# Optimization experiments

Hardware: AMD Instinct MI355X
Metric: run time of the kernel (lower is better)

## Reference

```python
import jax, jax.numpy as jnp
import numpy as np

COMMITMENT_COST = 0.25


def setup_inputs() -> dict:
    key = jax.random.key(0)
    k1, k2 = jax.random.split(key)
    ze = jax.random.normal(k1, (16, 256, 32, 32), dtype=jnp.float32)
    codebook = jax.random.normal(k2, (8192, 256), dtype=jnp.float32) * 0.02
    return {"ze": ze, "codebook": codebook}


def reference(ze, codebook):
    # ze: [B, C, H, W] -> [B, H, W, C]
    B, C, H, W = ze.shape
    ze_nhwc = jnp.transpose(ze, (0, 2, 3, 1))
    ze_flat = ze_nhwc.reshape(B * H * W, C)

    # squared L2 distances to every codebook row: [B*H*W, vocab]
    distances = (
        jnp.sum(ze_flat ** 2, axis=1, keepdims=True)
        + jnp.sum(codebook ** 2, axis=1)
        - 2.0 * ze_flat @ codebook.T
    )
    encoding_indices = jnp.argmin(distances, axis=1)  # [B*H*W]
    zq = codebook[encoding_indices].reshape(B, H, W, C)

    sg = jax.lax.stop_gradient
    quantization_loss = jnp.mean((sg(ze_nhwc) - zq) ** 2)
    commitment_loss = jnp.mean((ze_nhwc - sg(zq)) ** 2)
    vq_loss = quantization_loss + COMMITMENT_COST * commitment_loss

    # straight-through estimator (training mode)
    zq = ze_nhwc + sg(zq - ze_nhwc)
    zq = jnp.transpose(zq, (0, 3, 1, 2))  # back to [B, C, H, W]
    return vq_loss, zq, encoding_indices.reshape(B, H * W)
```

## Files before the change

### kernel.cpp

```cpp
#include <hip/hip_runtime.h>
#include <hip/hip_bf16.h>

#define NPIX 16384
#define NVOC 8192
#define CHUNK 32

typedef short short8v __attribute__((ext_vector_type(8)));
typedef float floatx4 __attribute__((ext_vector_type(4)));

#define WS_ZEBF   0u
#define WS_BLIST  0u
#define WS_PART   0u
#define WS_CBBF   8388608u
#define WS_PK     8388608u
#define WS_TAU    8519680u
#define WS_ZEF    12582912u
#define WS_MIN    29360128u
#define WS_BN     37748736u
#define WS_AN     37781504u
#define WS_BCNT   37847040u
#define WS_BMAXU  37847552u
#define WS_QCNT   37847556u
#define WS_QUEUE  37847808u

__device__ __forceinline__ short f2bf(float v) {
  __bf16 h = (__bf16)v;
  return __builtin_bit_cast(short, h);
}

__device__ __forceinline__ unsigned long long packdj(float d, int j) {
  return ((unsigned long long)__float_as_uint(d) << 32) | (unsigned int)j;
}

__device__ __forceinline__ void gll16(const void* g, void* l) {
  __builtin_amdgcn_global_load_lds(
      (const __attribute__((address_space(1))) void*)g,
      (__attribute__((address_space(3))) void*)l, 16, 0, 0);
}

__device__ __forceinline__ float np_pairwise128_sq(const float* x, int stride) {
  float r[8];
#pragma unroll
  for (int j = 0; j < 8; ++j) {
    float v = x[j * stride];
    r[j] = __fmul_rn(v, v);
  }
#pragma unroll
  for (int i = 1; i < 16; ++i) {
#pragma unroll
    for (int j = 0; j < 8; ++j) {
      float v = x[(i * 8 + j) * stride];
      r[j] = __fadd_rn(r[j], __fmul_rn(v, v));
    }
  }
  return __fadd_rn(__fadd_rn(__fadd_rn(r[0], r[1]), __fadd_rn(r[2], r[3])),
                   __fadd_rn(__fadd_rn(r[4], r[5]), __fadd_rn(r[6], r[7])));
}

__global__ __launch_bounds__(256) void k_bnorm(const float* __restrict__ cb,
                                               float* __restrict__ bn,
                                               unsigned* __restrict__ bmaxu) {
  __shared__ float rows[64][257];
  int tid = threadIdx.x;
  int c0 = blockIdx.x * 64;
  for (int r = 0; r < 64; ++r)
    rows[r][tid] = cb[(size_t)(c0 + r) * 256 + tid];
  __syncthreads();
  if (tid < 64) {
    float a = np_pairwise128_sq(&rows[tid][0], 1);
    float b = np_pairwise128_sq(&rows[tid][128], 1);
    float v = __fadd_rn(a, b);
    bn[c0 + tid] = v;
    atomicMax(bmaxu, __float_as_uint(v));
  }
}

__global__ __launch_bounds__(256) void k_cvt_ze(const float* __restrict__ ze,
                                                short* __restrict__ zebff,
                                                float* __restrict__ zef,
                                                float* __restrict__ an) {
  __shared__ float t[64][132];
  int tid = threadIdx.x;
  int p0 = blockIdx.x * 64;
  int b = p0 >> 10, hw0 = p0 & 1023;
  const float* src = ze + (size_t)b * 262144 + hw0;
  float apart = 0.f;
  for (int half = 0; half < 2; ++half) {
    if (half) __syncthreads();
    {
      int hw = tid & 63, cq = tid >> 6;
#pragma unroll
      for (int i = 0; i < 32; ++i) {
        int cl = i * 4 + cq;
        t[hw][cl] = src[(size_t)(half * 128 + cl) * 1024 + hw];
      }
    }
    __syncthreads();
    {
      int r = tid >> 2, cg = tid & 3;
      float* fd = zef + (size_t)(p0 + r) * 256 + half * 128 + cg * 32;
#pragma unroll
      for (int s = 0; s < 8; ++s) {
        float4 v = *reinterpret_cast<const float4*>(&t[r][cg * 32 + s * 4]);
        *reinterpret_cast<float4*>(fd + s * 4) = v;
      }
    }
    {
      int pg_l = tid >> 6, l = tid & 63;
      size_t pg = (size_t)(p0 >> 4) + pg_l;
      int lr = l & 15, lg = l >> 4;
#pragma unroll
      for (int kl = 0; kl < 4; ++kl) {
        int ks = half * 4 + kl;
        short8v v8;
#pragma unroll
        for (int e = 0; e < 8; ++e)
          v8[e] = f2bf(t[pg_l * 16 + lr][kl * 32 + lg * 8 + e]);
        *reinterpret_cast<short8v*>(zebff + (pg * 8 + ks) * 512 + l * 8) = v8;
      }
    }
    if (tid < 64) {
      float a = np_pairwise128_sq(&t[tid][0], 1);
      apart = half ? __fadd_rn(apart, a) : a;
    }
  }
  if (tid < 64) an[p0 + tid] = apart;
}

__global__ __launch_bounds__(256) void k_cvt_cb(const float* __restrict__ cb,
                                                short* __restrict__ cbbft,
                                                unsigned* __restrict__ bmaxu,
                                                int* __restrict__ qcnt) {
  __shared__ short t[64][264];
  int tid = threadIdx.x;
  if (blockIdx.x == 0 && tid == 0) {
    bmaxu[0] = 0u;
    qcnt[0] = 0;
  }
  int j0 = blockIdx.x * 64;
  {
    int col = tid >> 2, q = tid & 3;
    const float* src = cb + (size_t)(j0 + col) * 256 + q * 64;
#pragma unroll
    for (int i = 0; i < 8; ++i) {
      float4 a = *reinterpret_cast<const float4*>(src + i * 8);
      float4 b = *reinterpret_cast<const float4*>(src + i * 8 + 4);
      short8v v;
      v[0] = f2bf(a.x); v[1] = f2bf(a.y); v[2] = f2bf(a.z); v[3] = f2bf(a.w);
      v[4] = f2bf(b.x); v[5] = f2bf(b.y); v[6] = f2bf(b.z); v[7] = f2bf(b.w);
      *reinterpret_cast<short8v*>(&t[col][q * 64 + i * 8]) = v;
    }
  }
  __syncthreads();
  short* dst = cbbft + (size_t)blockIdx.x * 16384;
#pragma unroll
  for (int s = 0; s < 8; ++s) {
    int cid = tid + s * 256;
    int kc = cid >> 6, c2 = cid & 63;
    short8v v = *reinterpret_cast<const short8v*>(&t[c2][kc * 8]);
    *reinterpret_cast<short8v*>(dst + cid * 8) = v;
  }
}

__global__ __launch_bounds__(256, 2) void k_gemm(const short* __restrict__ zebff,
                                                 const short* __restrict__ cbbft,
                                                 const float* __restrict__ bn,
                                                 float* __restrict__ wsmin) {
  __shared__ short lds[32768];
  __shared__ float bnlds[1024];
  int tid = threadIdx.x;
  int lane = tid & 63, w = tid >> 6;
  int g = lane >> 4, r16 = lane & 15;
  int oct = blockIdx.x & 7, chunk = blockIdx.x >> 3;
  int p0 = chunk * 256;
  int ncol0 = oct * 1024;

  short8v pix[4][8];
  {
    const short* base = zebff + ((size_t)(p0 >> 4) + w * 4) * 4096 + lane * 8;
#pragma unroll
    for (int pf = 0; pf < 4; ++pf)
#pragma unroll
      for (int ks = 0; ks < 8; ++ks)
        pix[pf][ks] =
            *reinterpret_cast<const short8v*>(base + pf * 4096 + ks * 512);
  }
  gll16(bn + ncol0 + tid * 4, &bnlds[tid * 4]);

#define STAGE(t, boff)                                                         \
  {                                                                            \
    const short* src_ = cbbft + (size_t)(oct * 16 + (t)) * 16384;              \
    _Pragma("unroll") for (int s = 0; s < 8; ++s) {                            \
      int cid_ = tid + s * 256;                                                \
      gll16(src_ + cid_ * 8, &lds[(boff) + cid_ * 8]);                         \
    }                                                                          \
  }
  STAGE(0, 0)
  asm volatile("s_waitcnt vmcnt(0)" ::: "memory");
  __builtin_amdgcn_s_barrier();

  float* wbase = wsmin + (size_t)(oct * 16) * NPIX + p0 + w * 64 + r16;

  for (int t = 0; t < 16; ++t) {
    int bA = (t & 1) * 16384;
    int bC = bA ^ 16384;
    if (t < 15) STAGE(t + 1, bC)
    float4 bnv[4];
#pragma unroll
    for (int cf = 0; cf < 4; ++cf)
      bnv[cf] =
          *reinterpret_cast<const float4*>(&bnlds[t * 64 + cf * 16 + g * 4]);
    floatx4 acc[4][4];
#pragma unroll
    for (int cf = 0; cf < 4; ++cf)
#pragma unroll
      for (int pf = 0; pf < 4; ++pf) acc[cf][pf] = floatx4{0.f, 0.f, 0.f, 0.f};
    __builtin_amdgcn_s_setprio(1);
#pragma unroll
    for (int ks = 0; ks < 8; ++ks) {
      short8v cfr[4];
#pragma unroll
      for (int cf = 0; cf < 4; ++cf)
        cfr[cf] = *reinterpret_cast<const short8v*>(
            &lds[bA + (((ks * 4 + g) * 64) + cf * 16 + r16) * 8]);
#pragma unroll
      for (int cf = 0; cf < 4; ++cf)
#pragma unroll
        for (int pf = 0; pf < 4; ++pf)
          acc[cf][pf] = __builtin_amdgcn_mfma_f32_16x16x32_bf16(
              cfr[cf], pix[pf][ks], acc[cf][pf], 0, 0, 0);
    }
    __builtin_amdgcn_s_setprio(0);
    float pmin[4];
#pragma unroll
    for (int pf = 0; pf < 4; ++pf) {
      float m_ = 3.4e38f;
#pragma unroll
      for (int cf = 0; cf < 4; ++cf)
#pragma unroll
        for (int rr = 0; rr < 4; ++rr)
          m_ = fminf(m_, __builtin_fmaf(-2.0f, acc[cf][pf][rr], bnv[cf][rr]));
      m_ = fminf(m_, __shfl_xor(m_, 16));
      m_ = fminf(m_, __shfl_xor(m_, 32));
      pmin[pf] = m_;
    }
    if (lane < 16) {
#pragma unroll
      for (int pf = 0; pf < 4; ++pf)
        wbase[(size_t)t * NPIX + pf * 16] = pmin[pf];
    }
    asm volatile("s_waitcnt vmcnt(0)" ::: "memory");
    __builtin_amdgcn_s_barrier();
  }
#undef STAGE
}

__global__ __launch_bounds__(256) void k_tau(const float* __restrict__ wsmin,
                                             const float* __restrict__ an,
                                             const unsigned* __restrict__ bmaxu,
                                             float* __restrict__ tau,
                                             unsigned long long* __restrict__ pk) {
  __shared__ float sm[4][64];
  int tid = threadIdx.x;
  int px = tid & 63, q = tid >> 6;
  int p = blockIdx.x * 64 + px;
  float m0 = 3.4e38f, m1 = 3.4e38f, m2 = 3.4e38f, m3 = 3.4e38f;
#pragma unroll
  for (int i = 0; i < 8; ++i) {
    int c = q * 32 + i * 4;
    m0 = fminf(m0, wsmin[(size_t)c * NPIX + p]);
    m1 = fminf(m1, wsmin[(size_t)(c + 1) * NPIX + p]);
    m2 = fminf(m2, wsmin[(size_t)(c + 2) * NPIX + p]);
    m3 = fminf(m3, wsmin[(size_t)(c + 3) * NPIX + p]);
  }
  sm[q][px] = fminf(fminf(m0, m1), fminf(m2, m3));
  __syncthreads();
  if (tid < 64) {
    float m = fminf(fminf(sm[0][tid], sm[1][tid]), fminf(sm[2][tid], sm[3][tid]));
    float bmaxf = sqrtf(__uint_as_float(bmaxu[0]));
    tau[p] = m + 0.017f * sqrtf(an[p]) * bmaxf + 2e-4f;
    pk[p] = ~0ull;
  }
}

__global__ __launch_bounds__(256) void k_compact(const float* __restrict__ wsmin,
                                                 const float* __restrict__ tau,
                                                 int* __restrict__ bcnt,
                                                 int* __restrict__ blist,
                                                 int* __restrict__ qcnt,
                                                 int* __restrict__ queue) {
  __shared__ int wbase[4];
  __shared__ int running;
  int c = blockIdx.x;
  const float* row = wsmin + (size_t)c * NPIX;
  int* dst = blist + (size_t)c * NPIX;
  int tid = threadIdx.x;
  int lane = tid & 63, wv = tid >> 6;
  if (tid == 0) running = 0;
  __syncthreads();
  for (int base = 0; base < NPIX; base += 256) {
    int p = base + tid;
    bool flag = row[p] <= tau[p];
    unsigned long long mask = __ballot(flag);
    int cnt = __popcll(mask);
    int pre = __popcll(mask & ((1ull << lane) - 1ull));
    if (lane == 0) wbase[wv] = cnt;
    __syncthreads();
    if (tid == 0) {
      int r = running;
#pragma unroll
      for (int w2 = 0; w2 < 4; ++w2) {
        int t = wbase[w2];
        wbase[w2] = r;
        r += t;
      }
      running = r;
    }
    __syncthreads();
    if (flag) dst[wbase[wv] + pre] = p;
    __syncthreads();
  }
  if (tid == 0) {
    int n = running;
    bcnt[c] = n;
    int nch = (n + CHUNK - 1) / CHUNK;
    if (nch > 0) {
      int q0 = atomicAdd(qcnt, nch);
      for (int i = 0; i < nch; ++i) queue[q0 + i] = c | (i << 16);
    }
  }
}

__global__ __launch_bounds__(256) void k_rescore_b(
    const float* __restrict__ zef, const float* __restrict__ cb,
    const float* __restrict__ an, const float* __restrict__ bn,
    const int* __restrict__ bcnt, const int* __restrict__ blist,
    const int* __restrict__ qcnt, const int* __restrict__ queue,
    unsigned long long* __restrict__ pk) {
  __shared__ float cst[64][257];
  __shared__ float zl[32][264];
  __shared__ int pidx[32];
  __shared__ float apx[32];
  int tid = threadIdx.x;
  int lane = tid & 63, wv = tid >> 6;
  int nq = qcnt[0];
  for (int qi = blockIdx.x; qi < nq; qi += 256) {
    int e = queue[qi];
    int c = e & 0xffff;
    int chunk = e >> 16;
    int n = bcnt[c];
    int base = chunk * CHUNK;
    int cnt_here = min(CHUNK, n - base);
    __syncthreads();
    {
      int col = tid >> 2, kq = tid & 3;
      const float* src = cb + (size_t)(c * 64 + col) * 256 + kq * 64;
#pragma unroll
      for (int i = 0; i < 16; ++i) {
        float4 v = *reinterpret_cast<const float4*>(src + i * 4);
        *reinterpret_cast<float4*>(&cst[col][kq * 64 + i * 4]) = v;
      }
    }
    {
      int px = tid >> 3, seg = tid & 7;
      int idx = base + min(px, cnt_here - 1);
      int p = blist[(size_t)c * NPIX + idx];
      const float* src = zef + (size_t)p * 256 + seg * 32;
#pragma unroll
      for (int i = 0; i < 8; ++i) {
        float4 v = *reinterpret_cast<const float4*>(src + i * 4);
        *reinterpret_cast<float4*>(&zl[px][seg * 32 + i * 4]) = v;
      }
      if (seg == 0) {
        pidx[px] = p;
        apx[px] = an[p];
      }
    }
    __syncthreads();
    int j_global = c * 64 + lane;
    float bnj = bn[j_global];
    float acc[8];
#pragma unroll
    for (int i = 0; i < 8; ++i) acc[i] = 0.f;
#pragma unroll 4
    for (int k4 = 0; k4 < 64; ++k4) {
      float4 cv = *reinterpret_cast<const float4*>(&cst[lane][k4 * 4]);
#pragma unroll
      for (int i = 0; i < 8; ++i) {
        float4 zv =
            *reinterpret_cast<const float4*>(&zl[wv * 8 + i][k4 * 4]);
        acc[i] = __builtin_fmaf(zv.x, cv.x, acc[i]);
        acc[i] = __builtin_fmaf(zv.y, cv.y, acc[i]);
        acc[i] = __builtin_fmaf(zv.z, cv.z, acc[i]);
        acc[i] = __builtin_fmaf(zv.w, cv.w, acc[i]);
      }
    }
#pragma unroll
    for (int i = 0; i < 8; ++i) {
      int px = wv * 8 + i;
      float d = __fsub_rn(__fadd_rn(apx[px], bnj), 2.0f * acc[i]);
      unsigned long long q = packdj(d, j_global);
#pragma unroll
      for (int off = 1; off < 64; off <<= 1) {
        unsigned long long q2 = __shfl_xor(q, off);
        q = q2 < q ? q2 : q;
      }
      if (lane == 0) atomicMin(&pk[pidx[px]], q);
    }
  }
}

__global__ __launch_bounds__(256) void k_gather(const float* __restrict__ ze,
                                                const float* __restrict__ cb,
                                                const unsigned long long* __restrict__ pk,
                                                float* __restrict__ out_zq,
                                                float* __restrict__ out_idx,
                                                float* __restrict__ part) {
  __shared__ float qrow[64][257];
  __shared__ int sidx[64];
  int tid = threadIdx.x;
  int p0 = blockIdx.x * 64;
  int b = p0 >> 10, hw0 = p0 & 1023;
  if (tid < 64) {
    int bi = (int)(unsigned int)(pk[p0 + tid] & 0xffffffffull);
    sidx[tid] = bi;
    out_idx[p0 + tid] = (float)bi;
  }
  __syncthreads();
  for (int r = 0; r < 64; ++r)
    qrow[r][tid] = cb[(size_t)sidx[r] * 256 + tid];
  __syncthreads();
  float lsum = 0.f;
  size_t zbase = (size_t)b * 262144 + hw0;
#pragma unroll 4
  for (int i = 0; i < 64; ++i) {
    int px = tid & 63;
    int c = i * 4 + (tid >> 6);
    float qv = qrow[px][c];
    size_t gi = zbase + (size_t)c * 1024 + px;
    float zev = ze[gi];
    out_zq[gi] = __fadd_rn(zev, __fsub_rn(qv, zev));
    float d = zev - qv;
    lsum = __builtin_fmaf(d, d, lsum);
  }
#pragma unroll
  for (int off = 32; off; off >>= 1) lsum += __shfl_xor(lsum, off, 64);
  __shared__ float wsum[4];
  if ((tid & 63) == 0) wsum[tid >> 6] = lsum;
  __syncthreads();
  if (tid == 0) part[blockIdx.x] = (wsum[0] + wsum[1]) + (wsum[2] + wsum[3]);
}

__global__ __launch_bounds__(256) void k_final(const float* __restrict__ part,
                                               float* __restrict__ out0) {
  int tid = threadIdx.x;
  float s = part[tid];
#pragma unroll
  for (int off = 32; off; off >>= 1) s += __shfl_xor(s, off, 64);
  __shared__ float wsum[4];
  if ((tid & 63) == 0) wsum[tid >> 6] = s;
  __syncthreads();
  if (tid == 0)
    out0[0] = 1.25f * ((wsum[0] + wsum[1]) + (wsum[2] + wsum[3])) / 4194304.0f;
}

extern "C" void kernel_launch(void* const* d_in, const int* in_sizes, int n_in,
                              void* d_out, int out_size, void* d_ws, size_t ws_size,
                              hipStream_t stream) {
  const float* ze = (const float*)d_in[0];
  const float* cb = (const float*)d_in[1];
  float* out = (float*)d_out;
  char* ws = (char*)d_ws;
  short* zebff = (short*)(ws + WS_ZEBF);
  short* cbbft = (short*)(ws + WS_CBBF);
  float* zef = (float*)(ws + WS_ZEF);
  float* bn = (float*)(ws + WS_BN);
  float* an = (float*)(ws + WS_AN);
  float* wsmin = (float*)(ws + WS_MIN);
  float* tau = (float*)(ws + WS_TAU);
  int* blist = (int*)(ws + WS_BLIST);
  int* bcnt = (int*)(ws + WS_BCNT);
  unsigned* bmaxu = (unsigned*)(ws + WS_BMAXU);
  int* qcnt = (int*)(ws + WS_QCNT);
  int* queue = (int*)(ws + WS_QUEUE);
  unsigned long long* pk = (unsigned long long*)(ws + WS_PK);
  float* part = (float*)(ws + WS_PART);
  float* out_loss = out;
  float* out_zq = out + 1;
  float* out_idx = out + 1 + 4194304;

  k_cvt_ze<<<256, 256, 0, stream>>>(ze, zebff, zef, an);
  k_cvt_cb<<<128, 256, 0, stream>>>(cb, cbbft, bmaxu, qcnt);
  k_bnorm<<<128, 256, 0, stream>>>(cb, bn, bmaxu);
  k_gemm<<<512, 256, 0, stream>>>(zebff, cbbft, bn, wsmin);
  k_tau<<<256, 256, 0, stream>>>(wsmin, an, bmaxu, tau, pk);
  k_compact<<<128, 256, 0, stream>>>(wsmin, tau, bcnt, blist, qcnt, queue);
  k_rescore_b<<<256, 256, 0, stream>>>(zef, cb, an, bn, bcnt, blist, qcnt,
                                       queue, pk);
  k_gather<<<256, 256, 0, stream>>>(ze, cb, pk, out_zq, out_idx, part);
  k_final<<<1, 256, 0, stream>>>(part, out_loss);
}
```

Before: 192.6 us.

## Split rescore work into 32-code halves with swizzled codebook and direct-to-LDS loads

Each compacted bucket chunk now becomes two queue entries covering 32 codes each, which doubles the number of rescore work items and blocks and halves per-thread accumulators. A new pre-kernel writes an XOR-swizzled copy of the codebook into the reused min-distance workspace, so rows can be staged into LDS without padding and still be read without bank conflicts. Global loads go through gll16 (global-to-LDS) with an explicit vmcnt wait, and launch bounds ask for two blocks per CU. The cost is an extra full codebook copy pass, plus reliance on the wsmin buffer being dead after compaction.

```diff
diff --git a/kernel.cpp b/kernel.cpp
--- a/kernel.cpp
+++ b/kernel.cpp
@@ -325,70 +325,80 @@
     bcnt[c] = n;
     int nch = (n + CHUNK - 1) / CHUNK;
     if (nch > 0) {
-      int q0 = atomicAdd(qcnt, nch);
-      for (int i = 0; i < nch; ++i) queue[q0 + i] = c | (i << 16);
-    }
-  }
-}
-
-__global__ __launch_bounds__(256) void k_rescore_b(
-    const float* __restrict__ zef, const float* __restrict__ cb,
+      int q0 = atomicAdd(qcnt, nch * 2);
+      for (int i = 0; i < nch; ++i) {
+        queue[q0 + 2 * i] = (2 * c) | (i << 16);
+        queue[q0 + 2 * i + 1] = (2 * c + 1) | (i << 16);
+      }
+    }
+  }
+}
+
+__global__ __launch_bounds__(256) void k_swz(const float* __restrict__ cb,
+                                             float* __restrict__ cbsw) {
+  int gid = blockIdx.x * 256 + threadIdx.x;
+  int j = gid >> 6, u = gid & 63;
+  const float4 v =
+      reinterpret_cast<const float4*>(cb)[(size_t)j * 64 + (u ^ (j & 7))];
+  reinterpret_cast<float4*>(cbsw)[(size_t)j * 64 + u] = v;
+}
+
+__global__ __launch_bounds__(256, 2) void k_rescore_b(
+    const float* __restrict__ zef, const float* __restrict__ cbsw,
     const float* __restrict__ an, const float* __restrict__ bn,
     const int* __restrict__ bcnt, const int* __restrict__ blist,
     const int* __restrict__ qcnt, const int* __restrict__ queue,
     unsigned long long* __restrict__ pk) {
-  __shared__ float cst[64][257];
-  __shared__ float zl[32][264];
+  __shared__ float zl[32 * 256];
+  __shared__ float cstf[32 * 256];
   __shared__ int pidx[32];
   __shared__ float apx[32];
   int tid = threadIdx.x;
   int lane = tid & 63, wv = tid >> 6;
+  int code32 = lane & 31, half = lane >> 5;
   int nq = qcnt[0];
-  for (int qi = blockIdx.x; qi < nq; qi += 256) {
+  for (int qi = blockIdx.x; qi < nq; qi += 512) {
     int e = queue[qi];
-    int c = e & 0xffff;
-    int chunk = e >> 16;
+    int g = e & 0xffff, chunk = e >> 16;
+    int c = g >> 1;
     int n = bcnt[c];
     int base = chunk * CHUNK;
     int cnt_here = min(CHUNK, n - base);
     __syncthreads();
-    {
-      int col = tid >> 2, kq = tid & 3;
-      const float* src = cb + (size_t)(c * 64 + col) * 256 + kq * 64;
-#pragma unroll
-      for (int i = 0; i < 16; ++i) {
-        float4 v = *reinterpret_cast<const float4*>(src + i * 4);
-        *reinterpret_cast<float4*>(&cst[col][kq * 64 + i * 4]) = v;
-      }
-    }
-    {
-      int px = tid >> 3, seg = tid & 7;
+#pragma unroll
+    for (int i = 0; i < 8; ++i) {
+      int px = wv * 8 + i;
       int idx = base + min(px, cnt_here - 1);
       int p = blist[(size_t)c * NPIX + idx];
-      const float* src = zef + (size_t)p * 256 + seg * 32;
-#pragma unroll
-      for (int i = 0; i < 8; ++i) {
-        float4 v = *reinterpret_cast<const float4*>(src + i * 4);
-        *reinterpret_cast<float4*>(&zl[px][seg * 32 + i * 4]) = v;
-      }
-      if (seg == 0) {
-        pidx[px] = p;
-        apx[px] = an[p];
-      }
-    }
+      gll16(zef + (size_t)p * 256 + lane * 4, &zl[px * 256 + lane * 4]);
+    }
+#pragma unroll
+    for (int i = 0; i < 8; ++i) {
+      int r = wv * 8 + i;
+      gll16(cbsw + (size_t)(g * 32 + r) * 256 + lane * 4,
+            &cstf[r * 256 + lane * 4]);
+    }
+    if (tid < 32) {
+      int idx = base + min(tid, cnt_here - 1);
+      int p = blist[(size_t)c * NPIX + idx];
+      pidx[tid] = p;
+      apx[tid] = an[p];
+    }
+    asm volatile("s_waitcnt vmcnt(0)" ::: "memory");
     __syncthreads();
-    int j_global = c * 64 + lane;
-    float bnj = bn[j_global];
-    float acc[8];
-#pragma unroll
-    for (int i = 0; i < 8; ++i) acc[i] = 0.f;
-#pragma unroll 4
+    int jg = g * 32 + code32;
+    float bnj = bn[jg];
+    int px0 = wv * 8 + half * 4;
+    int sw = code32 & 7;
+    const float* crow = &cstf[code32 * 256];
+    float acc[4] = {0.f, 0.f, 0.f, 0.f};
+#pragma unroll 8
     for (int k4 = 0; k4 < 64; ++k4) {
-      float4 cv = *reinterpret_cast<const float4*>(&cst[lane][k4 * 4]);
-#pragma unroll
-      for (int i = 0; i < 8; ++i) {
+      float4 cv = *reinterpret_cast<const float4*>(&crow[(k4 ^ sw) << 2]);
+#pragma unroll
+      for (int i = 0; i < 4; ++i) {
         float4 zv =
-            *reinterpret_cast<const float4*>(&zl[wv * 8 + i][k4 * 4]);
+            *reinterpret_cast<const float4*>(&zl[(px0 + i) * 256 + k4 * 4]);
         acc[i] = __builtin_fmaf(zv.x, cv.x, acc[i]);
         acc[i] = __builtin_fmaf(zv.y, cv.y, acc[i]);
         acc[i] = __builtin_fmaf(zv.z, cv.z, acc[i]);
@@ -396,16 +406,16 @@
       }
     }
 #pragma unroll
-    for (int i = 0; i < 8; ++i) {
-      int px = wv * 8 + i;
+    for (int i = 0; i < 4; ++i) {
+      int px = px0 + i;
       float d = __fsub_rn(__fadd_rn(apx[px], bnj), 2.0f * acc[i]);
-      unsigned long long q = packdj(d, j_global);
-#pragma unroll
-      for (int off = 1; off < 64; off <<= 1) {
+      unsigned long long q = packdj(d, jg);
+#pragma unroll
+      for (int off = 1; off < 32; off <<= 1) {
         unsigned long long q2 = __shfl_xor(q, off);
         q = q2 < q ? q2 : q;
       }
-      if (lane == 0) atomicMin(&pk[pidx[px]], q);
+      if (code32 == 0) atomicMin(&pk[pidx[px]], q);
     }
   }
 }
@@ -477,6 +487,7 @@
   float* bn = (float*)(ws + WS_BN);
   float* an = (float*)(ws + WS_AN);
   float* wsmin = (float*)(ws + WS_MIN);
+  float* cbsw = (float*)(ws + WS_MIN);
   float* tau = (float*)(ws + WS_TAU);
   int* blist = (int*)(ws + WS_BLIST);
   int* bcnt = (int*)(ws + WS_BCNT);
@@ -495,7 +506,8 @@
   k_gemm<<<512, 256, 0, stream>>>(zebff, cbbft, bn, wsmin);
   k_tau<<<256, 256, 0, stream>>>(wsmin, an, bmaxu, tau, pk);
   k_compact<<<128, 256, 0, stream>>>(wsmin, tau, bcnt, blist, qcnt, queue);
-  k_rescore_b<<<256, 256, 0, stream>>>(zef, cb, an, bn, bcnt, blist, qcnt,
+  k_swz<<<2048, 256, 0, stream>>>(cb, cbsw);
+  k_rescore_b<<<512, 256, 0, stream>>>(zef, cbsw, an, bn, bcnt, blist, qcnt,
                                        queue, pk);
   k_gather<<<256, 256, 0, stream>>>(ze, cb, pk, out_zq, out_idx, part);
   k_final<<<1, 256, 0, stream>>>(part, out_loss);
```

Result: faster. 180.5 us (-6.3%).
